# Kernel tuning notes

Hardware: AMD Instinct MI355X
Metric: run time of the kernel (lower is better)

The kernel has to match this reference:

```python
import jax, jax.numpy as jnp
import numpy as np

FEAT = 1433
HID = 2
NUM_CLASS = 7
EPS = 1e-5  # torch BatchNorm1d default eps


def _bn_softsign(h, gamma, beta):
    # BatchNorm1d in training mode: batch stats over (batch, length) per channel.
    mu = h.mean(axis=(0, 2), keepdims=True)
    var = h.var(axis=(0, 2), keepdims=True)  # biased, matches torch normalization
    hn = (h - mu) * jax.lax.rsqrt(var + EPS)
    hn = hn * gamma[None, :, None] + beta[None, :, None]
    return hn / (1.0 + jnp.abs(hn))  # Softsign


def feature_adjacency(x, y):
    # (x.unsqueeze(-1) * y.unsqueeze(-2)).sum(dim=1) with x channel dim == 1
    # reduces to an outer product of x[:,0] with neighbor.sum over K.
    adj = jnp.einsum('bf,bg->bfg', x.sum(1), y.sum(1))  # [B,F,F]
    adj = adj + jnp.swapaxes(adj, -1, -2)
    adj = jnp.sqrt(adj)
    # row_normalize: divide by sum over dim 1, zero out inf/nan
    norm = adj / adj.sum(axis=1, keepdims=True)
    norm = jnp.where(jnp.isfinite(norm), norm, 0.0)
    return norm + jnp.eye(FEAT, dtype=x.dtype)


def featbrd(x, adj, W, b):
    # adjacency-based feature conv: y[b,c,f] = sum_g adj[(b),f,g] x[b,c,g],
    # then 1x1 conv over channels (Conv1d kernel_size=1).
    if adj.shape[0] == 1:
        y = jnp.einsum('fg,bcg->bcf', adj[0], x)
    else:
        y = jnp.einsum('bfg,bcg->bcf', adj, x)
    return jnp.einsum('oc,bcf->bof', W, y) + b[None, :, None]


def setup_inputs() -> dict:
    key = jax.random.key(0)
    ks = jax.random.split(key, 10)
    B, K = 64, 8
    inp = {
        'x': jax.random.uniform(ks[0], (B, 1, FEAT), dtype=jnp.float32),
        'neighbor': jax.random.uniform(ks[1], (B, K, FEAT), dtype=jnp.float32),
        'adj_buf': jnp.zeros((1, FEAT, FEAT), jnp.float32),
        'W1': jax.random.normal(ks[2], (HID, 1), jnp.float32) * 0.5,
        'b1': jnp.zeros((HID,), jnp.float32),
        'W2': jax.random.normal(ks[3], (HID, HID), jnp.float32) * 0.5,
        'b2': jnp.zeros((HID,), jnp.float32),
        'g1': jnp.ones((HID,), jnp.float32),
        'be1': jnp.zeros((HID,), jnp.float32),
        'g2': jnp.ones((HID,), jnp.float32),
        'be2': jnp.zeros((HID,), jnp.float32),
        'Wc': jax.random.normal(ks[4], (NUM_CLASS, FEAT * HID), jnp.float32) * 0.02,
        'bc': jnp.zeros((NUM_CLASS,), jnp.float32),
    }
    return inp


def reference(x, neighbor, adj_buf, W1, b1, W2, b2, g1, be1, g2, be2, Wc, bc):
    fadj = feature_adjacency(x, neighbor)          # [B,F,F]
    adj_tot = adj_buf + fadj.sum(0)                # [1,F,F] (buffer starts at zero)
    h = _bn_softsign(featbrd(x, fadj, W1, b1), g1, be1)      # [B,HID,F]
    h = _bn_softsign(featbrd(h, adj_tot, W2, b2), g2, be2)   # [B,HID,F]
    flat = h.reshape(h.shape[0], -1)               # Flatten (C then F, row-major)
    return flat @ Wc.T + bc
```

## Files before the change

kernel.cpp:

```cpp
#include <hip/hip_runtime.h>
#include <hip/hip_bf16.h>
#include <math.h>

constexpr int F   = 1433;
constexpr int NB  = 64;
constexpr int KN  = 8;
constexpr int BF  = NB * F;
constexpr float EPS = 1e-5f;

constexpr int SF  = 8;
constexpr int CH  = (F + SF - 1) / SF;
constexpr int SK  = 4;
constexpr int KCH = (F + SK - 1) / SK;
constexpr int FT  = 16;

constexpr int O_YS  = 0;
constexpr int O_BIG = O_YS + BF;
constexpr int O_P   = O_BIG + 8 * BF;
constexpr int O_Y1  = O_P + 4 * BF;
constexpr int O_HT  = O_Y1 + BF;
constexpr int O_Y2  = O_HT + 128 * F;
constexpr int O_AB  = O_Y2 + 2 * BF;
constexpr int O_ST  = O_AB + 1026752;

__global__ __launch_bounds__(256) void k_ys(const float* __restrict__ nb,
                                            float* __restrict__ ys) {
  int i = blockIdx.x * 256 + threadIdx.x;
  if (i >= BF) return;
  int b = i / F, g = i - b * F;
  const float* p = nb + (size_t)b * KN * F + g;
  float s = 0.f;
#pragma unroll
  for (int k = 0; k < KN; ++k) s += p[k * F];
  ys[i] = s;
}

__global__ __launch_bounds__(256) void k_D(const float* __restrict__ x,
                                           const float* __restrict__ ys,
                                           float* __restrict__ DP) {
  __shared__ __align__(16) float2 xy[CH];
  const int b = blockIdx.x, s = blockIdx.y;
  const int cs = s * CH, ce = min(cs + CH, F), cn = ce - cs;
  for (int i = threadIdx.x; i < cn; i += 256)
    xy[i] = make_float2(x[b * F + cs + i], ys[b * F + cs + i]);
  __syncthreads();
  float gx[6], gy[6], acc[6] = {};
#pragma unroll
  for (int j = 0; j < 6; ++j) {
    int g = threadIdx.x + 256 * j;
    gx[j] = (g < F) ? x[b * F + g] : 0.f;
    gy[j] = (g < F) ? ys[b * F + g] : 0.f;
  }
  for (int i = 0; i < cn; ++i) {
    float2 p = xy[i];
#pragma unroll
    for (int j = 0; j < 6; ++j)
      acc[j] += __builtin_amdgcn_sqrtf(fmaf(gy[j], p.x, gx[j] * p.y));
  }
#pragma unroll
  for (int j = 0; j < 6; ++j) {
    int g = threadIdx.x + 256 * j;
    if (g < F) DP[(size_t)s * BF + b * F + g] = acc[j];
  }
}

__global__ __launch_bounds__(256) void k_pack(const float* __restrict__ x,
                                              const float* __restrict__ ys,
                                              const float* __restrict__ DP,
                                              float4* __restrict__ P) {
  int i = blockIdx.x * 256 + threadIdx.x;
  if (i >= BF) return;
  float d = 0.f;
#pragma unroll
  for (int s = 0; s < SF; ++s) d += DP[(size_t)s * BF + i];
  float inv = (d > 0.f) ? 1.f / d : 0.f;
  P[i] = make_float4(x[i], ys[i], x[i] * inv, inv);
}

__global__ __launch_bounds__(256) void k_y1(const float4* __restrict__ P,
                                            float* __restrict__ Y1P) {
  __shared__ __align__(16) float4 pl[CH];
  const int b = blockIdx.x, s = blockIdx.y;
  const int cs = s * CH, ce = min(cs + CH, F), cn = ce - cs;
  for (int i = threadIdx.x; i < cn; i += 256) pl[i] = P[b * F + cs + i];
  __syncthreads();
  float fx[6], fy[6], acc[6] = {};
#pragma unroll
  for (int j = 0; j < 6; ++j) {
    int f = threadIdx.x + 256 * j;
    float4 p = (f < F) ? P[b * F + f] : make_float4(0.f, 0.f, 0.f, 0.f);
    fx[j] = p.x; fy[j] = p.y;
  }
  for (int i = 0; i < cn; ++i) {
    float4 p = pl[i];
#pragma unroll
    for (int j = 0; j < 6; ++j)
      acc[j] = fmaf(__builtin_amdgcn_sqrtf(fmaf(fx[j], p.y, fy[j] * p.x)), p.z, acc[j]);
  }
#pragma unroll
  for (int j = 0; j < 6; ++j) {
    int f = threadIdx.x + 256 * j;
    if (f < F) Y1P[(size_t)s * BF + b * F + f] = acc[j];
  }
}

__global__ __launch_bounds__(256) void k_A(const float* __restrict__ x,
                                           const float* __restrict__ ys,
                                           const float4* __restrict__ P,
                                           __hip_bfloat16* __restrict__ Ab) {
  __shared__ float2 fxy[FT][NB];
  const int fbase = blockIdx.y * FT;
  for (int i = threadIdx.x; i < FT * NB; i += 256) {
    int b = i >> 4, j = i & 15;
    int f = fbase + j;
    float vx = 0.f, vy = 0.f;
    if (f < F) { vx = x[b * F + f]; vy = ys[b * F + f]; }
    fxy[j][b] = make_float2(vx, vy);
  }
  __syncthreads();
  const int g = blockIdx.x * 256 + threadIdx.x;
  if (g >= F) return;
  float acc[FT] = {};
  for (int b = 0; b < NB; ++b) {
    float4 p = P[b * F + g];
#pragma unroll
    for (int j = 0; j < FT; ++j) {
      float2 w = fxy[j][b];
      acc[j] = fmaf(__builtin_amdgcn_sqrtf(fmaf(w.x, p.y, p.x * w.y)), p.w, acc[j]);
    }
  }
#pragma unroll
  for (int j = 0; j < FT; ++j) {
    int f = fbase + j;
    if (f < F) Ab[(size_t)f * F + g] = __float2bfloat16(acc[j]);
  }
}

__global__ __launch_bounds__(256) void k_stats1(const float4* __restrict__ P,
                                                const float* __restrict__ Y1P,
                                                float* __restrict__ y1,
                                                float* __restrict__ st) {
  float s = 0.f, sq = 0.f;
  for (int i = blockIdx.x * 256 + threadIdx.x; i < BF; i += gridDim.x * 256) {
    float v = P[i].x;
#pragma unroll
    for (int k = 0; k < SF; ++k) v += Y1P[(size_t)k * BF + i];
    y1[i] = v;
    s += v; sq += v * v;
  }
#pragma unroll
  for (int o = 32; o; o >>= 1) {
    s += __shfl_down(s, o, 64);
    sq += __shfl_down(sq, o, 64);
  }
  __shared__ float ls[4], lq[4];
  int wave = threadIdx.x >> 6, lane = threadIdx.x & 63;
  if (lane == 0) { ls[wave] = s; lq[wave] = sq; }
  __syncthreads();
  if (threadIdx.x == 0) {
    atomicAdd(&st[0], ls[0] + ls[1] + ls[2] + ls[3]);
    atomicAdd(&st[1], lq[0] + lq[1] + lq[2] + lq[3]);
  }
}

__global__ __launch_bounds__(256) void k_h1(const float* __restrict__ y1,
                                            const float* __restrict__ st,
                                            const float* __restrict__ W1,
                                            const float* __restrict__ g1,
                                            const float* __restrict__ be1,
                                            float* __restrict__ Ht,
                                            float* __restrict__ y2) {
  float mu = st[0] / (float)BF;
  float var = st[1] / (float)BF - mu * mu;
  float wa = W1[0], wb = W1[1];
  float k0 = wa * g1[0] / sqrtf(wa * wa * var + EPS);
  float k1 = wb * g1[1] / sqrtf(wb * wb * var + EPS);
  float c0 = -k0 * mu + be1[0];
  float c1 = -k1 * mu + be1[1];

  __shared__ float H[16][132];
  const int f0 = blockIdx.x * 16;
#pragma unroll
  for (int r = 0; r < 4; ++r) {
    int idx = threadIdx.x + r * 256;
    int b = idx >> 4, ff = idx & 15;
    int f = f0 + ff;
    float v = (f < F) ? y1[b * F + f] : 0.f;
    float h0 = fmaf(k0, v, c0); h0 = h0 / (1.f + fabsf(h0));
    float h1 = fmaf(k1, v, c1); h1 = h1 / (1.f + fabsf(h1));
    H[ff][2 * b] = h0;
    H[ff][2 * b + 1] = h1;
  }
  __syncthreads();
#pragma unroll
  for (int r = 0; r < 2; ++r) {
    int idx = threadIdx.x + r * 256;
    int ff = idx >> 5, c4 = (idx & 31) * 4;
    int f = f0 + ff;
    if (f < F) *(float4*)&Ht[f * 128 + c4] = *(const float4*)&H[ff][c4];
  }
#pragma unroll
  for (int r = 0; r < 8; ++r) {
    int idx = threadIdx.x + r * 256;
    int m = idx >> 4, ff = idx & 15;
    int f = f0 + ff;
    if (f < F) y2[m * F + f] = 64.f * H[ff][m];
  }
}

struct Pref { ushort a[4]; float4 h[4]; };

__device__ __forceinline__ void loadRegs(const ushort* __restrict__ Ab,
                                         const float* __restrict__ Ht,
                                         int f0, int ffs, int g4s, int tid,
                                         int gc, Pref& p) {
  int f = min(f0 + ffs, F - 1);
#pragma unroll
  for (int k = 0; k < 4; ++k) {
    int g = min(gc + g4s + k, F - 1);
    p.a[k] = Ab[(size_t)f * F + g];
  }
#pragma unroll
  for (int r = 0; r < 4; ++r) {
    int idx = tid + 256 * r;
    int gi = idx >> 5, c4 = (idx & 31) << 2;
    int g = min(gc + gi, F - 1);
    p.h[r] = *(const float4*)&Ht[g * 128 + c4];
  }
}

__device__ __forceinline__ void storeLDS(float* __restrict__ Al, float* __restrict__ Hl,
                                         int f0, int ffs, int g4s, int tid,
                                         int gc, int ge, const Pref& p) {
  bool fv = (f0 + ffs) < F;
#pragma unroll
  for (int k = 0; k < 4; ++k) {
    int g = gc + g4s + k;
    float v = 0.f;
    if (fv && g < ge) {
      __hip_bfloat16 bb = *(const __hip_bfloat16*)&p.a[k];
      v = __bfloat162float(bb);
    }
    Al[(g4s + k) * 36 + ffs] = v;
  }
#pragma unroll
  for (int r = 0; r < 4; ++r) {
    int idx = tid + 256 * r;
    int gi = idx >> 5, c4 = (idx & 31) << 2;
    float4 h = p.h[r];
    if (gc + gi >= ge) h = make_float4(0.f, 0.f, 0.f, 0.f);
    *(float4*)&Hl[gi * 132 + c4] = h;
  }
}

__global__ __launch_bounds__(256) void k_gemm(const ushort* __restrict__ Ab,
                                              const float* __restrict__ Ht,
                                              float* __restrict__ G2P) {
  __shared__ __align__(16) float Al[2][32 * 36];
  __shared__ __align__(16) float Hl[2][32 * 132];
  const int f0 = blockIdx.x * 32;
  const int gs = blockIdx.y * KCH;
  const int ge = min(gs + KCH, F);
  const int tid = threadIdx.x;
  const int ffs = tid >> 3;
  const int g4s = (tid & 7) * 4;
  const int fsub = (tid & 7) * 4;
  const int msub = (tid >> 3) * 4;
  float acc[4][4] = {};
  const int nch = (ge - gs + 31) >> 5;

  Pref p;
  loadRegs(Ab, Ht, f0, ffs, g4s, tid, gs, p);
  storeLDS(Al[0], Hl[0], f0, ffs, g4s, tid, gs, ge, p);
  __syncthreads();

  for (int c = 0; c < nch; ++c) {
    const int buf = c & 1;
    const bool more = (c + 1 < nch);
    if (more) loadRegs(Ab, Ht, f0, ffs, g4s, tid, gs + (c + 1) * 32, p);
    const float* Ab_ = Al[buf];
    const float* Hb_ = Hl[buf];
#pragma unroll 4
    for (int gi = 0; gi < 32; ++gi) {
      float4 a4 = *(const float4*)&Ab_[gi * 36 + fsub];
      float4 h4 = *(const float4*)&Hb_[gi * 132 + msub];
      float av[4] = {a4.x, a4.y, a4.z, a4.w};
      float hv[4] = {h4.x, h4.y, h4.z, h4.w};
#pragma unroll
      for (int i = 0; i < 4; ++i)
#pragma unroll
        for (int j = 0; j < 4; ++j)
          acc[i][j] = fmaf(av[i], hv[j], acc[i][j]);
    }
    if (more) storeLDS(Al[buf ^ 1], Hl[buf ^ 1], f0, ffs, g4s, tid, gs + (c + 1) * 32, ge, p);
    __syncthreads();
  }

  float* dst = G2P + (size_t)blockIdx.y * 128 * F;
#pragma unroll
  for (int i = 0; i < 4; ++i) {
    int f = f0 + fsub + i;
    if (f < F) {
#pragma unroll
      for (int j = 0; j < 4; ++j)
        dst[(msub + j) * F + f] = acc[i][j];
    }
  }
}

__global__ __launch_bounds__(256) void k_stats2(float* __restrict__ y2,
                                                const float* __restrict__ G2P,
                                                float* __restrict__ st) {
  float su = 0.f, sv = 0.f, suu = 0.f, svv = 0.f, suv = 0.f;
  for (int i = blockIdx.x * 256 + threadIdx.x; i < BF; i += gridDim.x * 256) {
    int b = i / F, f = i - b * F;
    int iu = (2 * b) * F + f, iv = iu + F;
    float u = y2[iu], v = y2[iv];
#pragma unroll
    for (int s = 0; s < SK; ++s) {
      u += G2P[(size_t)s * 128 * F + iu];
      v += G2P[(size_t)s * 128 * F + iv];
    }
    y2[iu] = u; y2[iv] = v;
    su += u; sv += v; suu += u * u; svv += v * v; suv += u * v;
  }
#pragma unroll
  for (int o = 32; o; o >>= 1) {
    su += __shfl_down(su, o, 64);
    sv += __shfl_down(sv, o, 64);
    suu += __shfl_down(suu, o, 64);
    svv += __shfl_down(svv, o, 64);
    suv += __shfl_down(suv, o, 64);
  }
  __shared__ float red[5][4];
  int wave = threadIdx.x >> 6, lane = threadIdx.x & 63;
  if (lane == 0) {
    red[0][wave] = su; red[1][wave] = sv; red[2][wave] = suu;
    red[3][wave] = svv; red[4][wave] = suv;
  }
  __syncthreads();
  if (threadIdx.x == 0) {
    atomicAdd(&st[2], red[0][0] + red[0][1] + red[0][2] + red[0][3]);
    atomicAdd(&st[3], red[1][0] + red[1][1] + red[1][2] + red[1][3]);
    atomicAdd(&st[4], red[2][0] + red[2][1] + red[2][2] + red[2][3]);
    atomicAdd(&st[5], red[3][0] + red[3][1] + red[3][2] + red[3][3]);
    atomicAdd(&st[6], red[4][0] + red[4][1] + red[4][2] + red[4][3]);
  }
}

__global__ __launch_bounds__(256) void k_out(const float* __restrict__ y2,
                                             const float* __restrict__ st,
                                             const float* __restrict__ W2,
                                             const float* __restrict__ b2,
                                             const float* __restrict__ g2,
                                             const float* __restrict__ be2,
                                             const float* __restrict__ Wc,
                                             const float* __restrict__ bc,
                                             float* __restrict__ out) {
  float n = (float)BF;
  float Eu = st[2] / n, Ev = st[3] / n;
  float Euu = st[4] / n, Evv = st[5] / n, Euv = st[6] / n;
  float cA[2], cB[2], cC[2];
#pragma unroll
  for (int o = 0; o < 2; ++o) {
    float w0 = W2[o * 2 + 0], w1 = W2[o * 2 + 1];
    float mean = w0 * Eu + w1 * Ev + b2[o];
    float Eh2 = w0 * w0 * Euu + 2.f * w0 * w1 * Euv + w1 * w1 * Evv +
                2.f * b2[o] * (w0 * Eu + w1 * Ev) + b2[o] * b2[o];
    float var = Eh2 - mean * mean;
    float inv = g2[o] / sqrtf(var + EPS);
    cA[o] = w0 * inv;
    cB[o] = w1 * inv;
    cC[o] = (b2[o] - mean) * inv + be2[o];
  }
  const int b = blockIdx.x;
  float acc[7] = {};
  for (int f = threadIdx.x; f < F; f += 256) {
    float u = y2[(2 * b) * F + f], v = y2[(2 * b + 1) * F + f];
    float h0 = fmaf(cA[0], u, fmaf(cB[0], v, cC[0]));
    h0 = h0 / (1.f + fabsf(h0));
    float h1 = fmaf(cA[1], u, fmaf(cB[1], v, cC[1]));
    h1 = h1 / (1.f + fabsf(h1));
#pragma unroll
    for (int o = 0; o < 7; ++o) acc[o] = fmaf(Wc[o * (2 * F) + f], h0, acc[o]);
#pragma unroll
    for (int o = 0; o < 7; ++o) acc[o] = fmaf(Wc[o * (2 * F) + F + f], h1, acc[o]);
  }
#pragma unroll
  for (int o = 0; o < 7; ++o) {
#pragma unroll
    for (int s = 32; s; s >>= 1) acc[o] += __shfl_down(acc[o], s, 64);
  }
  __shared__ float red[7][4];
  int wave = threadIdx.x >> 6, lane = threadIdx.x & 63;
  if (lane == 0) {
#pragma unroll
    for (int o = 0; o < 7; ++o) red[o][wave] = acc[o];
  }
  __syncthreads();
  if (threadIdx.x < 7) {
    int o = threadIdx.x;
    out[b * 7 + o] = red[o][0] + red[o][1] + red[o][2] + red[o][3] + bc[o];
  }
}

extern "C" void kernel_launch(void* const* d_in, const int* in_sizes, int n_in,
                              void* d_out, int out_size, void* d_ws, size_t ws_size,
                              hipStream_t stream) {
  const float* x    = (const float*)d_in[0];
  const float* nb   = (const float*)d_in[1];
  const float* W1   = (const float*)d_in[3];
  const float* W2   = (const float*)d_in[5];
  const float* b2   = (const float*)d_in[6];
  const float* g1   = (const float*)d_in[7];
  const float* be1  = (const float*)d_in[8];
  const float* g2   = (const float*)d_in[9];
  const float* be2  = (const float*)d_in[10];
  const float* Wc   = (const float*)d_in[11];
  const float* bc   = (const float*)d_in[12];
  float* out = (float*)d_out;
  float* ws = (float*)d_ws;

  float*  ys  = ws + O_YS;
  float*  BIG = ws + O_BIG;
  float4* P   = (float4*)(ws + O_P);
  float*  y1  = ws + O_Y1;
  float*  Ht  = ws + O_HT;
  float*  y2  = ws + O_Y2;
  __hip_bfloat16* Ab = (__hip_bfloat16*)(ws + O_AB);
  float*  st  = ws + O_ST;

  hipMemsetAsync(st, 0, 64 * sizeof(float), stream);

  k_ys    <<<(BF + 255) / 256, 256, 0, stream>>>(nb, ys);
  k_D     <<<dim3(NB, SF), 256, 0, stream>>>(x, ys, BIG);
  k_pack  <<<(BF + 255) / 256, 256, 0, stream>>>(x, ys, BIG, P);
  k_y1    <<<dim3(NB, SF), 256, 0, stream>>>(P, BIG);
  k_A     <<<dim3(6, (F + FT - 1) / FT), 256, 0, stream>>>(x, ys, P, Ab);
  k_stats1<<<128, 256, 0, stream>>>(P, BIG, y1, st);
  k_h1    <<<(F + 15) / 16, 256, 0, stream>>>(y1, st, W1, g1, be1, Ht, y2);
  k_gemm  <<<dim3((F + 31) / 32, SK), 256, 0, stream>>>((const ushort*)Ab, Ht, BIG);
  k_stats2<<<128, 256, 0, stream>>>(y2, BIG, st);
  k_out   <<<NB, 256, 0, stream>>>(y2, st, W2, b2, g2, be2, Wc, bc, out);
}
```

Measured before the change: 219.8 us.

## Fuse neighbor sum and normalizer pack into adjacent kernels, double split factors

Removes the k_ys and k_pack launches. The neighbor sum over K is now computed inside k_D, which stages the full x/ys row in shared memory. The inverse row-normalizer is computed inside k_y1, and only a scalar q array is written instead of the float4 P buffer. The split factors SF and SK are doubled, giving more blocks for the O(F^2) kernels and the GEMM, at the cost of more partial sums to reduce and redundant neighbor summing across the SF blocks of each batch row.

```diff
diff --git a/kernel.cpp b/kernel.cpp
--- a/kernel.cpp
+++ b/kernel.cpp
@@ -8,51 +8,49 @@
 constexpr int BF  = NB * F;
 constexpr float EPS = 1e-5f;
 
-constexpr int SF  = 8;
+constexpr int SF  = 16;
 constexpr int CH  = (F + SF - 1) / SF;
-constexpr int SK  = 4;
+constexpr int SK  = 8;
 constexpr int KCH = (F + SK - 1) / SK;
 constexpr int FT  = 16;
 
 constexpr int O_YS  = 0;
-constexpr int O_BIG = O_YS + BF;
-constexpr int O_P   = O_BIG + 8 * BF;
-constexpr int O_Y1  = O_P + 4 * BF;
+constexpr int O_Q   = O_YS + BF;
+constexpr int O_DP  = O_Q + BF;
+constexpr int O_Y1P = O_DP + SF * BF;
+constexpr int O_Y1  = O_Y1P + SF * BF;
 constexpr int O_HT  = O_Y1 + BF;
 constexpr int O_Y2  = O_HT + 128 * F;
 constexpr int O_AB  = O_Y2 + 2 * BF;
 constexpr int O_ST  = O_AB + 1026752;
 
-__global__ __launch_bounds__(256) void k_ys(const float* __restrict__ nb,
-                                            float* __restrict__ ys) {
-  int i = blockIdx.x * 256 + threadIdx.x;
-  if (i >= BF) return;
-  int b = i / F, g = i - b * F;
-  const float* p = nb + (size_t)b * KN * F + g;
-  float s = 0.f;
-#pragma unroll
-  for (int k = 0; k < KN; ++k) s += p[k * F];
-  ys[i] = s;
-}
-
 __global__ __launch_bounds__(256) void k_D(const float* __restrict__ x,
-                                           const float* __restrict__ ys,
-                                           float* __restrict__ DP) {
-  __shared__ __align__(16) float2 xy[CH];
+                                           const float* __restrict__ nbr,
+                                           float* __restrict__ DP,
+                                           float* __restrict__ ys_out) {
+  __shared__ __align__(16) float2 xy[F];
   const int b = blockIdx.x, s = blockIdx.y;
-  const int cs = s * CH, ce = min(cs + CH, F), cn = ce - cs;
-  for (int i = threadIdx.x; i < cn; i += 256)
-    xy[i] = make_float2(x[b * F + cs + i], ys[b * F + cs + i]);
-  __syncthreads();
+  for (int i = threadIdx.x; i < F; i += 256) {
+    const float* p = nbr + (size_t)b * KN * F + i;
+    float acc = 0.f;
+#pragma unroll
+    for (int k = 0; k < KN; ++k) acc += p[k * F];
+    xy[i] = make_float2(x[b * F + i], acc);
+  }
+  __syncthreads();
+  if (s == 0) {
+    for (int i = threadIdx.x; i < F; i += 256) ys_out[b * F + i] = xy[i].y;
+  }
+  const int cs = s * CH, cn = min(CH, F - cs);
   float gx[6], gy[6], acc[6] = {};
 #pragma unroll
   for (int j = 0; j < 6; ++j) {
     int g = threadIdx.x + 256 * j;
-    gx[j] = (g < F) ? x[b * F + g] : 0.f;
-    gy[j] = (g < F) ? ys[b * F + g] : 0.f;
+    float2 p = (g < F) ? xy[g] : make_float2(0.f, 0.f);
+    gx[j] = p.x; gy[j] = p.y;
   }
   for (int i = 0; i < cn; ++i) {
-    float2 p = xy[i];
+    float2 p = xy[cs + i];
 #pragma unroll
     for (int j = 0; j < 6; ++j)
       acc[j] += __builtin_amdgcn_sqrtf(fmaf(gy[j], p.x, gx[j] * p.y));
@@ -64,32 +62,31 @@
   }
 }
 
-__global__ __launch_bounds__(256) void k_pack(const float* __restrict__ x,
-                                              const float* __restrict__ ys,
-                                              const float* __restrict__ DP,
-                                              float4* __restrict__ P) {
-  int i = blockIdx.x * 256 + threadIdx.x;
-  if (i >= BF) return;
-  float d = 0.f;
-#pragma unroll
-  for (int s = 0; s < SF; ++s) d += DP[(size_t)s * BF + i];
-  float inv = (d > 0.f) ? 1.f / d : 0.f;
-  P[i] = make_float4(x[i], ys[i], x[i] * inv, inv);
-}
-
-__global__ __launch_bounds__(256) void k_y1(const float4* __restrict__ P,
-                                            float* __restrict__ Y1P) {
+__global__ __launch_bounds__(256) void k_y1(const float* __restrict__ x,
+                                            const float* __restrict__ ys,
+                                            const float* __restrict__ DP,
+                                            float* __restrict__ Y1P,
+                                            float* __restrict__ q) {
   __shared__ __align__(16) float4 pl[CH];
   const int b = blockIdx.x, s = blockIdx.y;
-  const int cs = s * CH, ce = min(cs + CH, F), cn = ce - cs;
-  for (int i = threadIdx.x; i < cn; i += 256) pl[i] = P[b * F + cs + i];
+  const int cs = s * CH, cn = min(CH, F - cs);
+  for (int i = threadIdx.x; i < cn; i += 256) {
+    int g = cs + i;
+    float d = 0.f;
+#pragma unroll
+    for (int t = 0; t < SF; ++t) d += DP[(size_t)t * BF + b * F + g];
+    float inv = (d > 0.f) ? 1.f / d : 0.f;
+    float xv = x[b * F + g], yv = ys[b * F + g];
+    pl[i] = make_float4(xv, yv, xv * inv, inv);
+    q[b * F + g] = inv;
+  }
   __syncthreads();
   float fx[6], fy[6], acc[6] = {};
 #pragma unroll
   for (int j = 0; j < 6; ++j) {
     int f = threadIdx.x + 256 * j;
-    float4 p = (f < F) ? P[b * F + f] : make_float4(0.f, 0.f, 0.f, 0.f);
-    fx[j] = p.x; fy[j] = p.y;
+    fx[j] = (f < F) ? x[b * F + f] : 0.f;
+    fy[j] = (f < F) ? ys[b * F + f] : 0.f;
   }
   for (int i = 0; i < cn; ++i) {
     float4 p = pl[i];
@@ -106,7 +103,7 @@
 
 __global__ __launch_bounds__(256) void k_A(const float* __restrict__ x,
                                            const float* __restrict__ ys,
-                                           const float4* __restrict__ P,
+                                           const float* __restrict__ q,
                                            __hip_bfloat16* __restrict__ Ab) {
   __shared__ float2 fxy[FT][NB];
   const int fbase = blockIdx.y * FT;
@@ -122,11 +119,11 @@
   if (g >= F) return;
   float acc[FT] = {};
   for (int b = 0; b < NB; ++b) {
-    float4 p = P[b * F + g];
+    float gx = x[b * F + g], gy = ys[b * F + g], gq = q[b * F + g];
 #pragma unroll
     for (int j = 0; j < FT; ++j) {
       float2 w = fxy[j][b];
-      acc[j] = fmaf(__builtin_amdgcn_sqrtf(fmaf(w.x, p.y, p.x * w.y)), p.w, acc[j]);
+      acc[j] = fmaf(__builtin_amdgcn_sqrtf(fmaf(w.x, gy, gx * w.y)), gq, acc[j]);
     }
   }
 #pragma unroll
@@ -136,13 +133,13 @@
   }
 }
 
-__global__ __launch_bounds__(256) void k_stats1(const float4* __restrict__ P,
+__global__ __launch_bounds__(256) void k_stats1(const float* __restrict__ x,
                                                 const float* __restrict__ Y1P,
                                                 float* __restrict__ y1,
                                                 float* __restrict__ st) {
   float s = 0.f, sq = 0.f;
   for (int i = blockIdx.x * 256 + threadIdx.x; i < BF; i += gridDim.x * 256) {
-    float v = P[i].x;
+    float v = x[i];
 #pragma unroll
     for (int k = 0; k < SF; ++k) v += Y1P[(size_t)k * BF + i];
     y1[i] = v;
@@ -408,7 +405,7 @@
                               void* d_out, int out_size, void* d_ws, size_t ws_size,
                               hipStream_t stream) {
   const float* x    = (const float*)d_in[0];
-  const float* nb   = (const float*)d_in[1];
+  const float* nbr  = (const float*)d_in[1];
   const float* W1   = (const float*)d_in[3];
   const float* W2   = (const float*)d_in[5];
   const float* b2   = (const float*)d_in[6];
@@ -421,25 +418,24 @@
   float* out = (float*)d_out;
   float* ws = (float*)d_ws;
 
-  float*  ys  = ws + O_YS;
-  float*  BIG = ws + O_BIG;
-  float4* P   = (float4*)(ws + O_P);
-  float*  y1  = ws + O_Y1;
-  float*  Ht  = ws + O_HT;
-  float*  y2  = ws + O_Y2;
+  float* ys  = ws + O_YS;
+  float* q   = ws + O_Q;
+  float* DP  = ws + O_DP;
+  float* Y1P = ws + O_Y1P;
+  float* y1  = ws + O_Y1;
+  float* Ht  = ws + O_HT;
+  float* y2  = ws + O_Y2;
   __hip_bfloat16* Ab = (__hip_bfloat16*)(ws + O_AB);
-  float*  st  = ws + O_ST;
+  float* st  = ws + O_ST;
 
   hipMemsetAsync(st, 0, 64 * sizeof(float), stream);
 
-  k_ys    <<<(BF + 255) / 256, 256, 0, stream>>>(nb, ys);
-  k_D     <<<dim3(NB, SF), 256, 0, stream>>>(x, ys, BIG);
-  k_pack  <<<(BF + 255) / 256, 256, 0, stream>>>(x, ys, BIG, P);
-  k_y1    <<<dim3(NB, SF), 256, 0, stream>>>(P, BIG);
-  k_A     <<<dim3(6, (F + FT - 1) / FT), 256, 0, stream>>>(x, ys, P, Ab);
-  k_stats1<<<128, 256, 0, stream>>>(P, BIG, y1, st);
+  k_D     <<<dim3(NB, SF), 256, 0, stream>>>(x, nbr, DP, ys);
+  k_y1    <<<dim3(NB, SF), 256, 0, stream>>>(x, ys, DP, Y1P, q);
+  k_A     <<<dim3(6, (F + FT - 1) / FT), 256, 0, stream>>>(x, ys, q, Ab);
+  k_stats1<<<128, 256, 0, stream>>>(x, Y1P, y1, st);
   k_h1    <<<(F + 15) / 16, 256, 0, stream>>>(y1, st, W1, g1, be1, Ht, y2);
-  k_gemm  <<<dim3((F + 31) / 32, SK), 256, 0, stream>>>((const ushort*)Ab, Ht, BIG);
-  k_stats2<<<128, 256, 0, stream>>>(y2, BIG, st);
+  k_gemm  <<<dim3((F + 31) / 32, SK), 256, 0, stream>>>((const ushort*)Ab, Ht, DP);
+  k_stats2<<<128, 256, 0, stream>>>(y2, DP, st);
   k_out   <<<NB, 256, 0, stream>>>(y2, st, W2, b2, g2, be2, Wc, bc, out);
 }
```

Measured after the change: 213.5 us. 2.9% less time.
